# Kernel tuning notes

Hardware: AMD Instinct MI355X
Metric: run time of the kernel (lower is better)

The kernel has to match this reference:

```python
import jax, jax.numpy as jnp
import numpy as np

K_SIZE = 5
PAD = 2  # (dilation*(k-1)+1 - stride + 1)//2 with k=5, dil=1, stride=1
SAMPLE_NUM = 15
DEPTH_MAX = 192.0


def _gather_patches(x, sample_idx):
    """x: [B,C,H,W] -> [B,H,W,S,C]: values of the 5x5 local neighborhood at the
    SAMPLE_NUM sampled kernel positions (zero padding, matching nn.Unfold)."""
    B, C, H, W = x.shape
    xp = jnp.pad(x, ((0, 0), (0, 0), (PAD, PAD), (PAD, PAD)))
    slabs = []
    for i in range(SAMPLE_NUM):  # small fixed constant, not a data dim
        p = sample_idx[i]
        dy = p // K_SIZE
        dx = p % K_SIZE
        slabs.append(jax.lax.dynamic_slice(xp, (0, 0, dy, dx), (B, C, H, W)))
    pat = jnp.stack(slabs, axis=1)          # [B,S,C,H,W]
    return pat.transpose(0, 3, 4, 1, 2)     # [B,H,W,S,C]


def setup_inputs() -> dict:
    key = jax.random.key(0)
    k1, k2, k3, k4 = jax.random.split(key, 4)
    B, C, H, W = 2, 32, 240, 320
    depth = jax.random.uniform(k1, (B, 1, H, W), dtype=jnp.float32) * 200.0
    surface_normal = jax.random.normal(k2, (B, 3, H, W), dtype=jnp.float32)
    features = jax.random.normal(k3, (B, C, H, W), dtype=jnp.float32)
    guide_weight = jnp.ones((B, H, W, K_SIZE * K_SIZE), dtype=jnp.float32)
    sample_idx = jax.random.randint(k4, (SAMPLE_NUM,), 0, K_SIZE * K_SIZE, dtype=jnp.int32)
    return {"depth": depth, "surface_normal": surface_normal, "features": features,
            "guide_weight": guide_weight, "sample_idx": sample_idx}


def reference(depth, surface_normal, features, guide_weight, sample_idx):
    b, c, h, w = features.shape
    d = depth[:, 0]                                          # squeeze(1) -> [B,H,W]
    valid = ((d > 0) & (d < DEPTH_MAX)).astype(features.dtype)[:, None]  # [B,1,H,W]

    feat_s = _gather_patches(features, sample_idx)           # [B,H,W,S,C]
    norm_s = _gather_patches(surface_normal, sample_idx)     # [B,H,W,S,3]
    valid_s = _gather_patches(valid, sample_idx)[..., 0]     # [B,H,W,S]

    # Faithful to torch: surface_normal.view(b, h, w, 3) is a raw memory
    # reinterpretation, NOT a permute.
    center_n = jnp.reshape(surface_normal, (b, h, w, 3))
    diff = jnp.sqrt(jnp.sum((norm_s - center_n[:, :, :, None, :]) ** 2, axis=-1))
    # torch detaches via the cpu/numpy round-trip -> stop_gradient here
    normal_w = jax.lax.stop_gradient(jnp.exp(-0.5 * diff))   # [B,H,W,S]

    guide_s = jnp.take(guide_weight, sample_idx, axis=3)     # [B,H,W,S]

    fw = valid_s * normal_w * guide_s                        # both weight flags True
    fw = jax.nn.softmax(fw, axis=-1)
    out = jnp.sum(feat_s * fw[..., None], axis=3)            # [B,H,W,C]
    return (out.transpose(0, 3, 1, 2), features)
```

## Files before the change

### kernel.cpp

```cpp
#include <hip/hip_runtime.h>

#define K_SIZE 5
#define PAD 2
#define SAMPLE_NUM 15
#define DEPTH_MAX 192.0f

constexpr int B = 2, C = 32, H = 240, W = 320;
constexpr int HW  = H * W;
constexpr int BHW = B * HW;
constexpr int TOT = B * C * HW;
constexpr int PPB = 64;
constexpr int NBLK = BHW / PPB;
constexpr int XCHUNK = NBLK / 8;

constexpr int WROWS = 5;
constexpr int WCOLS = 68;
constexpr int SEGS  = WCOLS / 4;
constexpr int CH_STRIDE = WROWS * WCOLS;
constexpr int STAGE_TASKS = C * WROWS * SEGS;

typedef float float4a __attribute__((ext_vector_type(4), aligned(16)));
typedef float float4u __attribute__((ext_vector_type(4), aligned(4)));

__global__ __launch_bounds__(256) void adaptive_sample_fused(
    const float* __restrict__ depth,
    const float* __restrict__ sn,
    const float* __restrict__ features,
    const float* __restrict__ guide,
    const int*   __restrict__ sample_idx,
    float* __restrict__ out,
    float* __restrict__ feat_out)
{
    __shared__ __align__(16) float lds_f[C * CH_STRIDE];
    __shared__ __align__(16) float w_lds[SAMPLE_NUM][WCOLS];

    const int bid = blockIdx.x;
    const int blk = (bid & 7) * XCHUNK + (bid >> 3);

    const int t    = threadIdx.x;
    const int base = blk * PPB;
    const int b    = base / HW;
    const int pix0 = base - b * HW;
    const int y    = pix0 / W;
    const int x0   = pix0 - y * W;
    const int planeBase = b * C * HW;

    for (int i = t; i < STAGE_TASKS; i += 256) {
        int ch  = i / (WROWS * SEGS);
        int rem = i - ch * (WROWS * SEGS);
        int r   = rem / SEGS;
        int k   = rem - r * SEGS;
        int yy  = min(max(y - 2 + r, 0), H - 1);
        int flat = planeBase + ch * HW + yy * W + (x0 - 2 + k * 4);
        float4a v;
        if (flat >= 0 && flat <= TOT - 4) {
            float4u g = *(const float4u*)(features + flat);
            v = float4a{g.x, g.y, g.z, g.w};
        } else {
            #pragma unroll
            for (int j = 0; j < 4; ++j)
                v[j] = features[min(max(flat + j, 0), TOT - 1)];
        }
        *(float4a*)&lds_f[ch * CH_STRIDE + r * WCOLS + k * 4] = v;
    }

    {
        const int s  = t & 15;
        const int lq = t >> 4;
        const float* snb = sn + (size_t)b * 3 * HW;
        const float* db  = depth + (size_t)b * HW;

        const int pp = sample_idx[(s < SAMPLE_NUM) ? s : 0];
        const int dy = pp / K_SIZE - PAD;
        const int dx = pp - (pp / K_SIZE) * K_SIZE - PAD;

        #pragma unroll
        for (int kk = 0; kk < 4; ++kk) {
            const int lp  = kk * 16 + lq;
            const int x   = x0 + lp;
            const int pix = pix0 + lp;

            const int yy = y + dy, xx = x + dx;
            const bool inb = (s < SAMPLE_NUM) &&
                             (yy >= 0) && (yy < H) && (xx >= 0) && (xx < W);
            const int noff = min(max(yy, 0), H - 1) * W + min(max(xx, 0), W - 1);

            const float d   = db[noff];
            const int   o   = pix * 3;
            const float cn0 = snb[o], cn1 = snb[o + 1], cn2 = snb[o + 2];
            const float d0  = snb[noff]          - cn0;
            const float d1  = snb[HW + noff]     - cn1;
            const float d2  = snb[2 * HW + noff] - cn2;
            const float gv  = guide[((size_t)b * HW + pix) * 25 + pp];

            const float diff = sqrtf(d0 * d0 + d1 * d1 + d2 * d2);
            const bool  ok   = inb && (d > 0.0f) && (d < DEPTH_MAX);
            const float prew = ok ? __expf(-0.5f * diff) * gv : 0.0f;

            float m = prew;
            #pragma unroll
            for (int mask = 1; mask < 16; mask <<= 1)
                m = fmaxf(m, __shfl_xor(m, mask, 16));
            float e = (s < SAMPLE_NUM) ? __expf(prew - m) : 0.0f;
            float sum = e;
            #pragma unroll
            for (int mask = 1; mask < 16; mask <<= 1)
                sum += __shfl_xor(sum, mask, 16);

            if (s < SAMPLE_NUM)
                w_lds[s][lp] = inb ? (e / sum) : 0.0f;
        }
    }
    __syncthreads();

    {
        const int q  = t & 15;
        const int cs = t >> 4;

        float4a wv[SAMPLE_NUM];
        #pragma unroll
        for (int s = 0; s < SAMPLE_NUM; ++s)
            wv[s] = *(const float4a*)&w_lds[s][4 * q];

        #pragma unroll
        for (int half = 0; half < 2; ++half) {
            const int ch = half * 16 + cs;
            const float* fpl = &lds_f[ch * CH_STRIDE];

            float4a acc = {0.0f, 0.0f, 0.0f, 0.0f};
            #pragma unroll
            for (int s = 0; s < SAMPLE_NUM; ++s) {
                int pp = sample_idx[s];
                int dy = pp / K_SIZE - PAD;
                int dx = pp - (pp / K_SIZE) * K_SIZE - PAD;
                int rr  = dy + 2;
                int xi0 = 4 * q + dx + 2;
                float4u f4 = *(const float4u*)&fpl[rr * WCOLS + xi0];
                acc += wv[s] * float4a{f4.x, f4.y, f4.z, f4.w};
            }

            const int gflat = planeBase + ch * HW + pix0 + 4 * q;
            float4a pf = *(const float4a*)(features + gflat);
            *(float4a*)(out + gflat)      = acc;
            *(float4a*)(feat_out + gflat) = pf;
        }
    }
}

extern "C" void kernel_launch(void* const* d_in, const int* in_sizes, int n_in,
                              void* d_out, int out_size, void* d_ws, size_t ws_size,
                              hipStream_t stream) {
    const float* depth      = (const float*)d_in[0];
    const float* sn         = (const float*)d_in[1];
    const float* features   = (const float*)d_in[2];
    const float* guide      = (const float*)d_in[3];
    const int*   sample_idx = (const int*)d_in[4];

    float* out      = (float*)d_out;
    float* feat_out = (float*)d_out + (size_t)B * C * HW;

    adaptive_sample_fused<<<NBLK, 256, 0, stream>>>(
        depth, sn, features, guide, sample_idx, out, feat_out);
}
```

Measured before the change: 48.10 us.

## Drop LDS feature staging; gather features directly from global memory via cache

Removes the shared-memory staging of the 5-row feature window. Features are now read with unaligned vector loads straight from global memory, relying on L1/L2 to serve the overlapping neighborhood reuse. Pixels per block double to 128, each thread now accumulates four channels, and launch bounds request higher occupancy. Out-of-range neighbors are clamped, with a scalar fix-up path for the few edge pixels where the flat-index clamp would read the wrong element. The cost is more global and cache traffic per output in exchange for dropping the LDS fill and its barrier latency.

```diff
diff --git a/kernel.cpp b/kernel.cpp
--- a/kernel.cpp
+++ b/kernel.cpp
@@ -9,20 +9,14 @@
 constexpr int HW  = H * W;
 constexpr int BHW = B * HW;
 constexpr int TOT = B * C * HW;
-constexpr int PPB = 64;
+constexpr int PPB = 128;
 constexpr int NBLK = BHW / PPB;
 constexpr int XCHUNK = NBLK / 8;
-
-constexpr int WROWS = 5;
-constexpr int WCOLS = 68;
-constexpr int SEGS  = WCOLS / 4;
-constexpr int CH_STRIDE = WROWS * WCOLS;
-constexpr int STAGE_TASKS = C * WROWS * SEGS;
 
 typedef float float4a __attribute__((ext_vector_type(4), aligned(16)));
 typedef float float4u __attribute__((ext_vector_type(4), aligned(4)));
 
-__global__ __launch_bounds__(256) void adaptive_sample_fused(
+__global__ __launch_bounds__(256, 6) void adaptive_sample_fused(
     const float* __restrict__ depth,
     const float* __restrict__ sn,
     const float* __restrict__ features,
@@ -31,8 +25,7 @@
     float* __restrict__ out,
     float* __restrict__ feat_out)
 {
-    __shared__ __align__(16) float lds_f[C * CH_STRIDE];
-    __shared__ __align__(16) float w_lds[SAMPLE_NUM][WCOLS];
+    __shared__ __align__(16) float w_lds[SAMPLE_NUM][PPB];
 
     const int bid = blockIdx.x;
     const int blk = (bid & 7) * XCHUNK + (bid >> 3);
@@ -41,44 +34,23 @@
     const int base = blk * PPB;
     const int b    = base / HW;
     const int pix0 = base - b * HW;
-    const int y    = pix0 / W;
-    const int x0   = pix0 - y * W;
-    const int planeBase = b * C * HW;
 
-    for (int i = t; i < STAGE_TASKS; i += 256) {
-        int ch  = i / (WROWS * SEGS);
-        int rem = i - ch * (WROWS * SEGS);
-        int r   = rem / SEGS;
-        int k   = rem - r * SEGS;
-        int yy  = min(max(y - 2 + r, 0), H - 1);
-        int flat = planeBase + ch * HW + yy * W + (x0 - 2 + k * 4);
-        float4a v;
-        if (flat >= 0 && flat <= TOT - 4) {
-            float4u g = *(const float4u*)(features + flat);
-            v = float4a{g.x, g.y, g.z, g.w};
-        } else {
-            #pragma unroll
-            for (int j = 0; j < 4; ++j)
-                v[j] = features[min(max(flat + j, 0), TOT - 1)];
-        }
-        *(float4a*)&lds_f[ch * CH_STRIDE + r * WCOLS + k * 4] = v;
-    }
+    const float* snb = sn + (size_t)b * 3 * HW;
+    const float* db  = depth + (size_t)b * HW;
 
     {
         const int s  = t & 15;
         const int lq = t >> 4;
-        const float* snb = sn + (size_t)b * 3 * HW;
-        const float* db  = depth + (size_t)b * HW;
-
         const int pp = sample_idx[(s < SAMPLE_NUM) ? s : 0];
         const int dy = pp / K_SIZE - PAD;
         const int dx = pp - (pp / K_SIZE) * K_SIZE - PAD;
 
         #pragma unroll
-        for (int kk = 0; kk < 4; ++kk) {
+        for (int kk = 0; kk < 8; ++kk) {
             const int lp  = kk * 16 + lq;
-            const int x   = x0 + lp;
             const int pix = pix0 + lp;
+            const int y   = pix / W;
+            const int x   = pix - y * W;
 
             const int yy = y + dy, xx = x + dx;
             const bool inb = (s < SAMPLE_NUM) &&
@@ -114,35 +86,64 @@
     __syncthreads();
 
     {
-        const int q  = t & 15;
-        const int cs = t >> 4;
+        const int q    = t & 31;
+        const int grp  = t >> 5;
+        const int ch0  = grp * 4;
+        const int pixq = pix0 + 4 * q;
+        const int y    = pixq / W;
+        const int x    = pixq - y * W;
+        const int pb0  = (b * C + ch0) * HW;
 
-        float4a wv[SAMPLE_NUM];
+        float4a acc[4];
         #pragma unroll
-        for (int s = 0; s < SAMPLE_NUM; ++s)
-            wv[s] = *(const float4a*)&w_lds[s][4 * q];
+        for (int cc = 0; cc < 4; ++cc) acc[cc] = float4a{0.f, 0.f, 0.f, 0.f};
 
         #pragma unroll
-        for (int half = 0; half < 2; ++half) {
-            const int ch = half * 16 + cs;
-            const float* fpl = &lds_f[ch * CH_STRIDE];
+        for (int s = 0; s < SAMPLE_NUM; ++s) {
+            int pp = sample_idx[s];
+            int dy = pp / K_SIZE - PAD;
+            int dx = pp - (pp / K_SIZE) * K_SIZE - PAD;
+            int yy = min(max(y + dy, 0), H - 1);
+            int rb = yy * W + x + dx;
+            float4a w4 = *(const float4a*)&w_lds[s][4 * q];
+            #pragma unroll
+            for (int cc = 0; cc < 4; ++cc) {
+                int flat = pb0 + cc * HW + rb;
+                flat = min(max(flat, 0), TOT - 4);
+                float4u f4 = *(const float4u*)(features + flat);
+                acc[cc] += w4 * float4a{f4.x, f4.y, f4.z, f4.w};
+            }
+        }
 
-            float4a acc = {0.0f, 0.0f, 0.0f, 0.0f};
+        const bool fix = (pb0 == 0 && x == 0 && y <= 2) ||
+                         (pb0 + 3 * HW == (B * C - 1) * HW && x == W - 4 && y >= H - 3);
+        if (fix) {
             #pragma unroll
-            for (int s = 0; s < SAMPLE_NUM; ++s) {
-                int pp = sample_idx[s];
-                int dy = pp / K_SIZE - PAD;
-                int dx = pp - (pp / K_SIZE) * K_SIZE - PAD;
-                int rr  = dy + 2;
-                int xi0 = 4 * q + dx + 2;
-                float4u f4 = *(const float4u*)&fpl[rr * WCOLS + xi0];
-                acc += wv[s] * float4a{f4.x, f4.y, f4.z, f4.w};
+            for (int cc = 0; cc < 4; ++cc) {
+                const float* fpl = features + pb0 + cc * HW;
+                float a0 = 0, a1 = 0, a2 = 0, a3 = 0;
+                for (int s = 0; s < SAMPLE_NUM; ++s) {
+                    int pp = sample_idx[s];
+                    int dy = pp / K_SIZE - PAD;
+                    int dx = pp - (pp / K_SIZE) * K_SIZE - PAD;
+                    int yy = min(max(y + dy, 0), H - 1);
+                    const float* frow = fpl + yy * W;
+                    int xb = x + dx;
+                    a0 += w_lds[s][4 * q + 0] * frow[min(max(xb + 0, 0), W - 1)];
+                    a1 += w_lds[s][4 * q + 1] * frow[min(max(xb + 1, 0), W - 1)];
+                    a2 += w_lds[s][4 * q + 2] * frow[min(max(xb + 2, 0), W - 1)];
+                    a3 += w_lds[s][4 * q + 3] * frow[min(max(xb + 3, 0), W - 1)];
+                }
+                acc[cc] = float4a{a0, a1, a2, a3};
             }
+        }
 
-            const int gflat = planeBase + ch * HW + pix0 + 4 * q;
-            float4a pf = *(const float4a*)(features + gflat);
-            *(float4a*)(out + gflat)      = acc;
-            *(float4a*)(feat_out + gflat) = pf;
+        #pragma unroll
+        for (int cc = 0; cc < 4; ++cc) {
+            const int flat = pb0 + cc * HW + pixq;
+            float4a pf = *(const float4a*)(features + flat);
+            *(float4a*)(out + flat)      = acc[cc];
+            *(float4a*)(feat_out + flat) = pf;
         }
     }
 }
```

After: 47.98 us. Within noise of the previous version (-0.2%).
